# Kernel tuning notes

Hardware: AMD Instinct MI355X
Metric: run time of the kernel (lower is better)

## Reference

```python
import jax, jax.numpy as jnp
import numpy as np

HIDDEN = 1024


def setup_inputs() -> dict:
    key = jax.random.key(0)
    ks = jax.random.split(key, 8)
    x_in, y_in, out_dim, hidden = 1024, 1024, 1024, HIDDEN
    Nx, Ny = 4096, 4096
    s = lambda d: 1.0 / np.sqrt(d)
    return {
        "x": jax.random.normal(ks[0], (Nx, x_in), jnp.float32),
        "y": jax.random.normal(ks[1], (Ny, y_in), jnp.float32),
        "Wq": jax.random.normal(ks[2], (hidden, x_in), jnp.float32) * s(x_in),
        "bq": jnp.zeros((hidden,), jnp.float32),
        "Wk": jax.random.normal(ks[3], (hidden, y_in), jnp.float32) * s(y_in),
        "bk": jnp.zeros((hidden,), jnp.float32),
        "Wv": jax.random.normal(ks[4], (out_dim, y_in), jnp.float32) * s(y_in),
        "bv": jnp.zeros((out_dim,), jnp.float32),
    }


def reference(x, y, Wq, bq, Wk, bk, Wv, bv):
    # Linear projections (torch Linear: x @ W.T + b)
    q = x @ Wq.T + bq          # [Nx, H]
    k = y @ Wk.T + bk          # [Ny, H]
    v = y @ Wv.T + bv          # [Ny, D_out]
    scores = (q @ k.T) / jnp.sqrt(jnp.asarray(HIDDEN, q.dtype))  # [Nx, Ny]
    attn = jax.nn.softmax(scores, axis=1)
    return attn @ v            # [Nx, D_out]
```

## Files before the change

kernel.cpp:

```cpp
#include <hip/hip_runtime.h>
#include <cstdint>
#include <cstddef>

typedef __attribute__((ext_vector_type(8))) __bf16 bf16x8;
typedef __attribute__((ext_vector_type(4))) float  f32x4;

#define WAITCNT_VM(n)   ((n & 0xF) | 0x70 | 0xF00 | (((n) >> 4) << 14))
#define WAITCNT_LGKM(n) (0xF | 0x70 | ((n) << 8) | (3 << 14))

__device__ __forceinline__ unsigned short f32_to_bf16(float f) {
    union { float f; unsigned int u; } cv;
    cv.f = f;
    unsigned int u = cv.u;
    return (unsigned short)((u + 0x7fffu + ((u >> 16) & 1u)) >> 16);
}

__device__ __forceinline__ float bf16_to_f32(unsigned short h) {
    union { unsigned int u; float f; } cv;
    cv.u = ((unsigned int)h) << 16;
    return cv.f;
}

__device__ __forceinline__ void async_copy16(const unsigned short* g, unsigned short* lds) {
    __builtin_amdgcn_global_load_lds(
        (const __attribute__((address_space(1))) unsigned int*)g,
        (__attribute__((address_space(3))) unsigned int*)lds,
        16, 0, 0);
}

__global__ __launch_bounds__(256) void cast_all(
    const float* __restrict__ x,  const float* __restrict__ y,
    const float* __restrict__ wq, const float* __restrict__ wk, const float* __restrict__ wv,
    unsigned short* __restrict__ xb,  unsigned short* __restrict__ yb,
    unsigned short* __restrict__ wqb, unsigned short* __restrict__ wkb,
    unsigned short* __restrict__ wvb, float* __restrict__ lsum)
{
    int b = blockIdx.x;
    if (b >= 11264) {
        float4 z = {0.f, 0.f, 0.f, 0.f};
#pragma unroll
        for (int t = 0; t < 4; ++t)
            ((float4*)lsum)[threadIdx.x * 4 + t] = z;
        return;
    }
    const float* s; unsigned short* d; int base;
    if      (b < 4096)  { s = x;  d = xb;  base = b; }
    else if (b < 8192)  { s = y;  d = yb;  base = b - 4096; }
    else if (b < 9216)  { s = wq; d = wqb; base = b - 8192; }
    else if (b < 10240) { s = wk; d = wkb; base = b - 9216; }
    else                { s = wv; d = wvb; base = b - 10240; }
    int i = base * 256 + threadIdx.x;
    float4 v = ((const float4*)s)[i];
    ushort4 o;
    o.x = f32_to_bf16(v.x);
    o.y = f32_to_bf16(v.y);
    o.z = f32_to_bf16(v.z);
    o.w = f32_to_bf16(v.w);
    ((ushort4*)d)[i] = o;
}

__device__ __forceinline__ void gemm_core_pf(
    const unsigned short* __restrict__ A, const unsigned short* __restrict__ B,
    int K, int rowBase, int colBase, int kBeg, int kEnd,
    unsigned short* ldsA, unsigned short* ldsB, f32x4 acc[4][4])
{
    const int tid  = threadIdx.x;
    const int lane = tid & 63;
    const int wave = tid >> 6;
    const int quad = lane >> 4;
    const int r    = lane & 15;
    const int wm   = wave >> 1;
    const int wn   = wave & 1;

    const int c1 = tid + 256;
    const long aOff0 = (long)(rowBase + (tid >> 2)) * K + (tid & 3) * 8;
    const long aOff1 = (long)(rowBase + (c1  >> 2)) * K + (c1  & 3) * 8;
    const long bOff0 = (long)(colBase + (tid >> 2)) * K + (tid & 3) * 8;
    const long bOff1 = (long)(colBase + (c1  >> 2)) * K + (c1  & 3) * 8;
    unsigned short* ldsA0 = ldsA + tid * 8;
    unsigned short* ldsA1 = ldsA + c1 * 8;
    unsigned short* ldsB0 = ldsB + tid * 8;
    unsigned short* ldsB1 = ldsB + c1 * 8;

    const int aReadOff = (wm * 64 + r) * 32 + quad * 8;
    const int bReadOff = (wn * 64 + r) * 32 + quad * 8;

    const int nSteps = (kEnd - kBeg) >> 5;

    async_copy16(A + aOff0 + kBeg, ldsA0);
    async_copy16(A + aOff1 + kBeg, ldsA1);
    async_copy16(B + bOff0 + kBeg, ldsB0);
    async_copy16(B + bOff1 + kBeg, ldsB1);

    for (int s = 0; s < nSteps; ++s) {
        const int cur = (s & 1) << 12;
        const int nxt = cur ^ 4096;
        __builtin_amdgcn_s_waitcnt(0);
        __syncthreads();
        if (s + 1 < nSteps) {
            const int kn = kBeg + ((s + 1) << 5);
            async_copy16(A + aOff0 + kn, ldsA0 + nxt);
            async_copy16(A + aOff1 + kn, ldsA1 + nxt);
            async_copy16(B + bOff0 + kn, ldsB0 + nxt);
            async_copy16(B + bOff1 + kn, ldsB1 + nxt);
        }
        bf16x8 af[4], bfr[4];
#pragma unroll
        for (int i = 0; i < 4; ++i)
            af[i] = *(const bf16x8*)(ldsA + cur + aReadOff + i * 16 * 32);
#pragma unroll
        for (int j = 0; j < 4; ++j)
            bfr[j] = *(const bf16x8*)(ldsB + cur + bReadOff + j * 16 * 32);
#pragma unroll
        for (int i = 0; i < 4; ++i)
#pragma unroll
            for (int j = 0; j < 4; ++j)
                acc[i][j] = __builtin_amdgcn_mfma_f32_16x16x32_bf16(af[i], bfr[j], acc[i][j], 0, 0, 0);
    }
}

__global__ __launch_bounds__(256, 2)
void proj_batched(const unsigned short* __restrict__ xb, const unsigned short* __restrict__ yb,
                  const unsigned short* __restrict__ wqb, const unsigned short* __restrict__ wkb,
                  const unsigned short* __restrict__ wvb,
                  unsigned short* __restrict__ q, unsigned short* __restrict__ k,
                  unsigned short* __restrict__ vt,
                  const float* __restrict__ bq, const float* __restrict__ bk,
                  const float* __restrict__ bv)
{
    __shared__ __align__(16) unsigned short ldsA[2 * 128 * 32];
    __shared__ __align__(16) unsigned short ldsB[2 * 128 * 32];

    const int b = blockIdx.x;
    const int z = b >> 8;
    const int rb = b & 255;

    const unsigned short *A, *B;
    unsigned short* C;
    const float* bias;
    int N, rowBase, colBase;
    bool biasPerRow;
    if (z == 0) {
        A = xb; B = wqb; C = q; bias = bq; N = 1024; biasPerRow = false;
        colBase = (rb >> 5) * 128; rowBase = (rb & 31) * 128;
    } else if (z == 1) {
        A = yb; B = wkb; C = k; bias = bk; N = 1024; biasPerRow = false;
        colBase = (rb >> 5) * 128; rowBase = (rb & 31) * 128;
    } else {
        A = wvb; B = yb; C = vt; bias = bv; N = 4096; biasPerRow = true;
        colBase = (rb >> 3) * 128; rowBase = (rb & 7) * 128;
    }

    f32x4 acc[4][4];
#pragma unroll
    for (int i = 0; i < 4; ++i)
#pragma unroll
        for (int j = 0; j < 4; ++j)
            acc[i][j] = (f32x4){0.f, 0.f, 0.f, 0.f};

    gemm_core_pf(A, B, 1024, rowBase, colBase, 0, 1024, ldsA, ldsB, acc);

    const int lane = threadIdx.x & 63;
    const int wave = threadIdx.x >> 6;
    const int quad = lane >> 4;
    const int r    = lane & 15;
    const int orow0 = rowBase + (wave >> 1) * 64 + quad * 4;
    const int ocol0 = colBase + (wave & 1) * 64 + r;

#pragma unroll
    for (int i = 0; i < 4; ++i)
#pragma unroll
        for (int e = 0; e < 4; ++e) {
            const int row = orow0 + i * 16 + e;
            const float brow = biasPerRow ? bias[row] : 0.f;
#pragma unroll
            for (int j = 0; j < 4; ++j) {
                const int col = ocol0 + j * 16;
                const float bb = biasPerRow ? brow : bias[col];
                C[(long)row * N + col] = f32_to_bf16(acc[i][j][e] + bb);
            }
        }
}

__device__ __forceinline__ void stage_half(const unsigned short* src, long rstep,
                                           unsigned short* ldsLane) {
    async_copy16(src, ldsLane);
    async_copy16(src + rstep, ldsLane + 4096);
}

__device__ __forceinline__ void gemm256_core(
    const unsigned short* __restrict__ A, const unsigned short* __restrict__ B,
    int K, int rowBase, int colBase, int kBeg, int nTiles,
    unsigned short* lds, f32x4 acc[8][4])
{
    const int tid  = threadIdx.x;
    const int lane = tid & 63;
    const int wid  = tid >> 6;
    const int quad = lane >> 4;
    const int r    = lane & 15;
    const int wm   = wid >> 2;
    const int wn   = wid & 3;

    const int row0 = tid >> 3;
    const int chs8 = (((tid & 7) ^ (row0 & 7)) << 3);
    const unsigned short* As = A + (long)(rowBase + row0) * K + chs8 + kBeg;
    const unsigned short* Bs = B + (long)(colBase + row0) * K + chs8 + kBeg;
    const long rstep = (long)K * 64;
    const long hstep = (long)K * 128;
    unsigned short* ldsLane = lds + tid * 8;

    const int aRd = (wm << 13) + (r << 6);
    const int bRd = 16384 + (wn << 12) + (r << 6);
    const int sw0 = ((quad ^ (r & 7)) << 3);
    const int sw1 = (((quad + 4) ^ (r & 7)) << 3);

    stage_half(As,         rstep, ldsLane);
    stage_half(As + hstep, rstep, ldsLane + 8192);
    stage_half(Bs,         rstep, ldsLane + 16384);
    stage_half(Bs + hstep, rstep, ldsLane + 24576);
    if (nTiles > 1) {
        stage_half(Bs + 64,         rstep, ldsLane + 32768 + 16384);
        stage_half(Bs + hstep + 64, rstep, ldsLane + 32768 + 24576);
    }
    __builtin_amdgcn_s_waitcnt(WAITCNT_VM(4));
    __builtin_amdgcn_s_barrier();
    __builtin_amdgcn_sched_barrier(0);

    bf16x8 aE[4], aO[4], bX[4], bY[4];
#pragma unroll
    for (int i = 0; i < 4; ++i)
        aE[i] = *(const bf16x8*)(lds + aRd + i * 1024 + sw0);
#pragma unroll
    for (int j = 0; j < 4; ++j)
        bX[j] = *(const bf16x8*)(lds + bRd + j * 1024 + sw0);

    for (int T = 0; T < nTiles; ++T) {
        const int cur = (T & 1) << 15;
        const int nxt = cur ^ 32768;

#pragma unroll
        for (int i = 0; i < 4; ++i)
            aO[i] = *(const bf16x8*)(lds + cur + aRd + (4 + i) * 1024 + sw0);
        __builtin_amdgcn_s_waitcnt(WAITCNT_LGKM(4));
        __builtin_amdgcn_sched_barrier(0);
        __builtin_amdgcn_s_setprio(1);
#pragma unroll
        for (int i = 0; i < 4; ++i)
#pragma unroll
            for (int j = 0; j < 4; ++j)
                acc[i][j] = __builtin_amdgcn_mfma_f32_16x16x32_bf16(aE[i], bX[j], acc[i][j], 0, 0, 0);
        __builtin_amdgcn_s_setprio(0);
        __builtin_amdgcn_sched_barrier(0);
        __builtin_amdgcn_s_barrier();
        if (T + 1 < nTiles) stage_half(As + (T + 1) * 64, rstep, ldsLane + nxt);

#pragma unroll
        for (int i = 0; i < 4; ++i)
            aE[i] = *(const bf16x8*)(lds + cur + aRd + i * 1024 + sw1);
#pragma unroll
        for (int j = 0; j < 4; ++j)
            bY[j] = *(const bf16x8*)(lds + cur + bRd + j * 1024 + sw1);
        __builtin_amdgcn_s_waitcnt(WAITCNT_LGKM(8));
        __builtin_amdgcn_sched_barrier(0);
        __builtin_amdgcn_s_setprio(1);
#pragma unroll
        for (int i = 0; i < 4; ++i)
#pragma unroll
            for (int j = 0; j < 4; ++j)
                acc[4 + i][j] = __builtin_amdgcn_mfma_f32_16x16x32_bf16(aO[i], bX[j], acc[4 + i][j], 0, 0, 0);
        __builtin_amdgcn_s_setprio(0);
        __builtin_amdgcn_sched_barrier(0);
        __builtin_amdgcn_s_barrier();
        if (T + 1 < nTiles) stage_half(As + hstep + (T + 1) * 64, rstep, ldsLane + nxt + 8192);

#pragma unroll
        for (int i = 0; i < 4; ++i)
            aO[i] = *(const bf16x8*)(lds + cur + aRd + (4 + i) * 1024 + sw1);
        __builtin_amdgcn_s_waitcnt(WAITCNT_LGKM(4));
        __builtin_amdgcn_sched_barrier(0);
        __builtin_amdgcn_s_setprio(1);
#pragma unroll
        for (int i = 0; i < 4; ++i)
#pragma unroll
            for (int j = 0; j < 4; ++j)
                acc[i][j] = __builtin_amdgcn_mfma_f32_16x16x32_bf16(aE[i], bY[j], acc[i][j], 0, 0, 0);
        __builtin_amdgcn_s_setprio(0);
        __builtin_amdgcn_sched_barrier(0);
        __builtin_amdgcn_s_barrier();
        if (T + 2 < nTiles) stage_half(Bs + (T + 2) * 64, rstep, ldsLane + cur + 16384);

        if (T + 1 < nTiles) {
            if (T + 2 < nTiles) __builtin_amdgcn_s_waitcnt(WAITCNT_VM(2));
            else                __builtin_amdgcn_s_waitcnt(WAITCNT_VM(0));
            __builtin_amdgcn_s_barrier();
            __builtin_amdgcn_sched_barrier(0);
#pragma unroll
            for (int i = 0; i < 4; ++i)
                aE[i] = *(const bf16x8*)(lds + nxt + aRd + i * 1024 + sw0);
#pragma unroll
            for (int j = 0; j < 4; ++j)
                bX[j] = *(const bf16x8*)(lds + nxt + bRd + j * 1024 + sw0);
            __builtin_amdgcn_s_waitcnt(WAITCNT_LGKM(8));
        } else {
            __builtin_amdgcn_s_waitcnt(WAITCNT_LGKM(0));
        }
        __builtin_amdgcn_sched_barrier(0);
        __builtin_amdgcn_s_setprio(1);
#pragma unroll
        for (int i = 0; i < 4; ++i)
#pragma unroll
            for (int j = 0; j < 4; ++j)
                acc[4 + i][j] = __builtin_amdgcn_mfma_f32_16x16x32_bf16(aO[i], bY[j], acc[4 + i][j], 0, 0, 0);
        __builtin_amdgcn_s_setprio(0);
        __builtin_amdgcn_sched_barrier(0);
        if (T + 2 < nTiles) stage_half(Bs + hstep + (T + 2) * 64, rstep, ldsLane + cur + 24576);
    }
}

__global__ __launch_bounds__(512, 2)
void scores_gemm256(const unsigned short* __restrict__ q, const unsigned short* __restrict__ k,
                    unsigned short* __restrict__ P, float* __restrict__ lsum, float scale2)
{
    __shared__ __align__(16) unsigned short lds[2 * 32768];

    const int bid = blockIdx.x;
    const int swz = (bid & 7) * 32 + (bid >> 3);
    const int mt = swz >> 4, nt = swz & 15;
    const int rowBase = mt * 256;
    const int colBase = nt * 256;

    f32x4 acc[8][4];
#pragma unroll
    for (int i = 0; i < 8; ++i)
#pragma unroll
        for (int j = 0; j < 4; ++j)
            acc[i][j] = (f32x4){0.f, 0.f, 0.f, 0.f};

    gemm256_core(q, k, 1024, rowBase, colBase, 0, 16, lds, acc);

    const int lane = threadIdx.x & 63;
    const int wid  = threadIdx.x >> 6;
    const int quad = lane >> 4;
    const int r    = lane & 15;
    const int orow0 = rowBase + (wid >> 2) * 128 + quad * 4;
    const int ocol0 = colBase + (wid & 3) * 64 + r;

#pragma unroll
    for (int mi = 0; mi < 8; ++mi)
#pragma unroll
        for (int e = 0; e < 4; ++e) {
            const int row = orow0 + mi * 16 + e;
            float rs = 0.f;
#pragma unroll
            for (int nj = 0; nj < 4; ++nj) {
                const float p = exp2f(acc[mi][nj][e] * scale2);
                rs += p;
                P[(long)row * 4096 + ocol0 + nj * 16] = f32_to_bf16(p);
            }
#pragma unroll
            for (int m = 1; m < 16; m <<= 1) rs += __shfl_xor(rs, m, 64);
            if (r == 0) atomicAdd(&lsum[row], rs);
        }
}

template <int ATOMIC>
__global__ __launch_bounds__(512, 2)
void out_gemm256(const unsigned short* __restrict__ P, const unsigned short* __restrict__ vt,
                 void* __restrict__ Out)
{
    __shared__ __align__(16) unsigned short lds[2 * 32768];

    const int bid = blockIdx.x;
    const int swz = (bid & 7) * 32 + (bid >> 3);
    const int z  = swz & 3;
    const int nt = (swz >> 2) & 3;
    const int mt = swz >> 4;
    const int rowBase = mt * 256;
    const int colBase = nt * 256;
    const int kBeg = z * 1024;

    f32x4 acc[8][4];
#pragma unroll
    for (int i = 0; i < 8; ++i)
#pragma unroll
        for (int j = 0; j < 4; ++j)
            acc[i][j] = (f32x4){0.f, 0.f, 0.f, 0.f};

    gemm256_core(P, vt, 4096, rowBase, colBase, kBeg, 16, lds, acc);

    const int lane = threadIdx.x & 63;
    const int wid  = threadIdx.x >> 6;
    const int quad = lane >> 4;
    const int r    = lane & 15;
    const int orow0 = rowBase + (wid >> 2) * 128 + quad * 4;
    const int ocol0 = colBase + (wid & 3) * 64 + r;

#pragma unroll
    for (int mi = 0; mi < 8; ++mi)
#pragma unroll
        for (int e = 0; e < 4; ++e) {
            const int row = orow0 + mi * 16 + e;
#pragma unroll
            for (int nj = 0; nj < 4; ++nj) {
                const int col = ocol0 + nj * 16;
                if (ATOMIC) {
                    atomicAdd(&((float*)Out)[(long)row * 1024 + col], acc[mi][nj][e]);
                } else {
                    unsigned short* parts = (unsigned short*)Out + (size_t)z * (4096 * 1024);
                    parts[(long)row * 1024 + col] = f32_to_bf16(acc[mi][nj][e]);
                }
            }
        }
}

__global__ __launch_bounds__(256) void reduce_norm4(const unsigned short* __restrict__ parts,
                                                    const float* __restrict__ lsum,
                                                    float* __restrict__ O) {
    const int i = blockIdx.x * 256 + threadIdx.x;
    const float inv = 1.0f / lsum[i >> 8];
    const size_t stride = (size_t)(4096 * 1024) / 4;
    ushort4 a = ((const ushort4*)parts)[i];
    ushort4 b = ((const ushort4*)parts)[i + stride];
    ushort4 c = ((const ushort4*)parts)[i + 2 * stride];
    ushort4 d = ((const ushort4*)parts)[i + 3 * stride];
    float4 o;
    o.x = (bf16_to_f32(a.x) + bf16_to_f32(b.x) + bf16_to_f32(c.x) + bf16_to_f32(d.x)) * inv;
    o.y = (bf16_to_f32(a.y) + bf16_to_f32(b.y) + bf16_to_f32(c.y) + bf16_to_f32(d.y)) * inv;
    o.z = (bf16_to_f32(a.z) + bf16_to_f32(b.z) + bf16_to_f32(c.z) + bf16_to_f32(d.z)) * inv;
    o.w = (bf16_to_f32(a.w) + bf16_to_f32(b.w) + bf16_to_f32(c.w) + bf16_to_f32(d.w)) * inv;
    ((float4*)O)[i] = o;
}

__global__ __launch_bounds__(256) void norm_rows(float* __restrict__ O, const float* __restrict__ lsum) {
    int i = blockIdx.x * 256 + threadIdx.x;
    const float inv = 1.0f / lsum[i >> 8];
    float4 v = ((const float4*)O)[i];
    v.x *= inv; v.y *= inv; v.z *= inv; v.w *= inv;
    ((float4*)O)[i] = v;
}

extern "C" void kernel_launch(void* const* d_in, const int* in_sizes, int n_in,
                              void* d_out, int out_size, void* d_ws, size_t ws_size,
                              hipStream_t stream) {
    const float* x  = (const float*)d_in[0];
    const float* y  = (const float*)d_in[1];
    const float* Wq = (const float*)d_in[2];
    const float* bq = (const float*)d_in[3];
    const float* Wk = (const float*)d_in[4];
    const float* bk = (const float*)d_in[5];
    const float* Wv = (const float*)d_in[6];
    const float* bv = (const float*)d_in[7];

    constexpr int Nx = 4096, Ny = 4096, H = 1024, Dv = 1024, Kin = 1024;

    char* ws = (char*)d_ws;
    size_t off = 0;
    auto carve = [&](size_t bytes) {
        char* p = ws + off;
        off += (bytes + 255) & ~(size_t)255;
        return p;
    };

    unsigned short* q_bf  = (unsigned short*)carve((size_t)Nx * H * 2);
    unsigned short* k_bf  = (unsigned short*)carve((size_t)Ny * H * 2);
    unsigned short* vt_bf = (unsigned short*)carve((size_t)Dv * Ny * 2);
    float*          lsum  = (float*)carve((size_t)Nx * sizeof(float));

    char* overlay = ws + off;
    unsigned short* x_bf  = (unsigned short*)overlay;
    unsigned short* y_bf  = x_bf  + (size_t)Nx * Kin;
    unsigned short* Wq_bf = y_bf  + (size_t)Ny * Kin;
    unsigned short* Wk_bf = Wq_bf + (size_t)H  * Kin;
    unsigned short* Wv_bf = Wk_bf + (size_t)H  * Kin;
    unsigned short* P_bf  = (unsigned short*)overlay;

    const size_t overlay_bytes = (size_t)Nx * Ny * 2;
    const size_t partsBytes = (size_t)Nx * Dv * 2;
    unsigned short* parts = (unsigned short*)(overlay + overlay_bytes);
    const size_t need_parts = (size_t)((overlay + overlay_bytes + 4 * partsBytes) - ws);
    const bool useParts = ws_size >= need_parts;

    if (!useParts)
        hipMemsetAsync(d_out, 0, (size_t)Nx * Dv * sizeof(float), stream);

    cast_all<<<11265, 256, 0, stream>>>(x, y, Wq, Wk, Wv, x_bf, y_bf, Wq_bf, Wk_bf, Wv_bf, lsum);

    proj_batched<<<768, 256, 0, stream>>>(x_bf, y_bf, Wq_bf, Wk_bf, Wv_bf,
                                          q_bf, k_bf, vt_bf, bq, bk, bv);

    const float scale2 = 1.4426950408889634f / 32.0f;
    scores_gemm256<<<256, 512, 0, stream>>>(q_bf, k_bf, P_bf, lsum, scale2);

    if (useParts) {
        out_gemm256<0><<<256, 512, 0, stream>>>(P_bf, vt_bf, parts);
        reduce_norm4<<<(Nx * Dv / 4) / 256, 256, 0, stream>>>(parts, lsum, (float*)d_out);
    } else {
        out_gemm256<1><<<256, 512, 0, stream>>>(P_bf, vt_bf, d_out);
        norm_rows<<<Nx * Dv / 4 / 256, 256, 0, stream>>>((float*)d_out, lsum);
    }
}
```

Baseline: 223.1 us.

## Fuse split-K reduction and normalization into output GEMM via last-block counter

Removes the separate reduce_norm4 kernel. Each split-K block of the output GEMM writes its bf16 partial, then increments a per-tile atomic counter, and the last of the four blocks sums the partials, applies the row normalization and writes fp32 output. This saves one kernel launch and lets the reduction overlap with other tiles' GEMM work. In exchange it adds a memset for the counters, fences, and a serialized reduction tail in the last block of each tile.

```diff
diff --git a/kernel.cpp b/kernel.cpp
--- a/kernel.cpp
+++ b/kernel.cpp
@@ -182,13 +182,12 @@
         }
 }
 
-__device__ __forceinline__ void stage_half(const unsigned short* src, long rstep,
-                                           unsigned short* ldsLane) {
-    async_copy16(src, ldsLane);
-    async_copy16(src + rstep, ldsLane + 4096);
-}
-
-__device__ __forceinline__ void gemm256_core(
+#define G256_BAR  __builtin_amdgcn_s_barrier()
+#define G256_SB   __builtin_amdgcn_sched_barrier(0)
+#define G256_PR1  __builtin_amdgcn_s_setprio(1)
+#define G256_PR0  __builtin_amdgcn_s_setprio(0)
+
+__device__ __forceinline__ void gemm256_la(
     const unsigned short* __restrict__ A, const unsigned short* __restrict__ B,
     int K, int rowBase, int colBase, int kBeg, int nTiles,
     unsigned short* lds, f32x4 acc[8][4])
@@ -214,17 +213,22 @@
     const int sw0 = ((quad ^ (r & 7)) << 3);
     const int sw1 = (((quad + 4) ^ (r & 7)) << 3);
 
-    stage_half(As,         rstep, ldsLane);
-    stage_half(As + hstep, rstep, ldsLane + 8192);
-    stage_half(Bs,         rstep, ldsLane + 16384);
-    stage_half(Bs + hstep, rstep, ldsLane + 24576);
+    auto STG = [&](const unsigned short* src, int ldsOff) {
+        async_copy16(src,         ldsLane + ldsOff);
+        async_copy16(src + rstep, ldsLane + ldsOff + 4096);
+    };
+
+    STG(As,         0);
+    STG(As + hstep, 8192);
+    STG(Bs,         16384);
+    STG(Bs + hstep, 24576);
     if (nTiles > 1) {
-        stage_half(Bs + 64,         rstep, ldsLane + 32768 + 16384);
-        stage_half(Bs + hstep + 64, rstep, ldsLane + 32768 + 24576);
+        STG(Bs + 64,         32768 + 16384);
+        STG(Bs + hstep + 64, 32768 + 24576);
     }
     __builtin_amdgcn_s_waitcnt(WAITCNT_VM(4));
-    __builtin_amdgcn_s_barrier();
-    __builtin_amdgcn_sched_barrier(0);
+    G256_BAR;
+    G256_SB;
 
     bf16x8 aE[4], aO[4], bX[4], bY[4];
 #pragma unroll
@@ -242,17 +246,17 @@
         for (int i = 0; i < 4; ++i)
             aO[i] = *(const bf16x8*)(lds + cur + aRd + (4 + i) * 1024 + sw0);
         __builtin_amdgcn_s_waitcnt(WAITCNT_LGKM(4));
-        __builtin_amdgcn_sched_barrier(0);
-        __builtin_amdgcn_s_setprio(1);
+        G256_SB;
+        G256_PR1;
 #pragma unroll
         for (int i = 0; i < 4; ++i)
 #pragma unroll
             for (int j = 0; j < 4; ++j)
                 acc[i][j] = __builtin_amdgcn_mfma_f32_16x16x32_bf16(aE[i], bX[j], acc[i][j], 0, 0, 0);
-        __builtin_amdgcn_s_setprio(0);
-        __builtin_amdgcn_sched_barrier(0);
-        __builtin_amdgcn_s_barrier();
-        if (T + 1 < nTiles) stage_half(As + (T + 1) * 64, rstep, ldsLane + nxt);
+        G256_PR0;
+        G256_SB;
+        G256_BAR;
+        if (T + 1 < nTiles) STG(As + (T + 1) * 64, nxt);
 
 #pragma unroll
         for (int i = 0; i < 4; ++i)
@@ -261,39 +265,39 @@
         for (int j = 0; j < 4; ++j)
             bY[j] = *(const bf16x8*)(lds + cur + bRd + j * 1024 + sw1);
         __builtin_amdgcn_s_waitcnt(WAITCNT_LGKM(8));
-        __builtin_amdgcn_sched_barrier(0);
-        __builtin_amdgcn_s_setprio(1);
+        G256_SB;
+        G256_PR1;
 #pragma unroll
         for (int i = 0; i < 4; ++i)
 #pragma unroll
             for (int j = 0; j < 4; ++j)
                 acc[4 + i][j] = __builtin_amdgcn_mfma_f32_16x16x32_bf16(aO[i], bX[j], acc[4 + i][j], 0, 0, 0);
-        __builtin_amdgcn_s_setprio(0);
-        __builtin_amdgcn_sched_barrier(0);
-        __builtin_amdgcn_s_barrier();
-        if (T + 1 < nTiles) stage_half(As + hstep + (T + 1) * 64, rstep, ldsLane + nxt + 8192);
+        G256_PR0;
+        G256_SB;
+        G256_BAR;
+        if (T + 1 < nTiles) STG(As + hstep + (T + 1) * 64, nxt + 8192);
 
 #pragma unroll
         for (int i = 0; i < 4; ++i)
             aO[i] = *(const bf16x8*)(lds + cur + aRd + (4 + i) * 1024 + sw1);
         __builtin_amdgcn_s_waitcnt(WAITCNT_LGKM(4));
-        __builtin_amdgcn_sched_barrier(0);
-        __builtin_amdgcn_s_setprio(1);
+        G256_SB;
+        G256_PR1;
 #pragma unroll
         for (int i = 0; i < 4; ++i)
 #pragma unroll
             for (int j = 0; j < 4; ++j)
                 acc[i][j] = __builtin_amdgcn_mfma_f32_16x16x32_bf16(aE[i], bY[j], acc[i][j], 0, 0, 0);
-        __builtin_amdgcn_s_setprio(0);
-        __builtin_amdgcn_sched_barrier(0);
-        __builtin_amdgcn_s_barrier();
-        if (T + 2 < nTiles) stage_half(Bs + (T + 2) * 64, rstep, ldsLane + cur + 16384);
+        G256_PR0;
+        G256_SB;
+        G256_BAR;
+        if (T + 2 < nTiles) STG(Bs + (T + 2) * 64, cur + 16384);
 
         if (T + 1 < nTiles) {
             if (T + 2 < nTiles) __builtin_amdgcn_s_waitcnt(WAITCNT_VM(2));
             else                __builtin_amdgcn_s_waitcnt(WAITCNT_VM(0));
-            __builtin_amdgcn_s_barrier();
-            __builtin_amdgcn_sched_barrier(0);
+            G256_BAR;
+            G256_SB;
 #pragma unroll
             for (int i = 0; i < 4; ++i)
                 aE[i] = *(const bf16x8*)(lds + nxt + aRd + i * 1024 + sw0);
@@ -304,16 +308,16 @@
         } else {
             __builtin_amdgcn_s_waitcnt(WAITCNT_LGKM(0));
         }
-        __builtin_amdgcn_sched_barrier(0);
-        __builtin_amdgcn_s_setprio(1);
+        G256_SB;
+        G256_PR1;
 #pragma unroll
         for (int i = 0; i < 4; ++i)
 #pragma unroll
             for (int j = 0; j < 4; ++j)
                 acc[4 + i][j] = __builtin_amdgcn_mfma_f32_16x16x32_bf16(aO[i], bY[j], acc[4 + i][j], 0, 0, 0);
-        __builtin_amdgcn_s_setprio(0);
-        __builtin_amdgcn_sched_barrier(0);
-        if (T + 2 < nTiles) stage_half(Bs + hstep + (T + 2) * 64, rstep, ldsLane + cur + 24576);
+        G256_PR0;
+        G256_SB;
+        if (T + 2 < nTiles) STG(Bs + hstep + (T + 2) * 64, cur + 24576);
     }
 }
 
@@ -336,7 +340,7 @@
         for (int j = 0; j < 4; ++j)
             acc[i][j] = (f32x4){0.f, 0.f, 0.f, 0.f};
 
-    gemm256_core(q, k, 1024, rowBase, colBase, 0, 16, lds, acc);
+    gemm256_la(q, k, 1024, rowBase, colBase, 0, 16, lds, acc);
 
     const int lane = threadIdx.x & 63;
     const int wid  = threadIdx.x >> 6;
@@ -363,12 +367,13 @@
         }
 }
 
-template <int ATOMIC>
 __global__ __launch_bounds__(512, 2)
-void out_gemm256(const unsigned short* __restrict__ P, const unsigned short* __restrict__ vt,
-                 void* __restrict__ Out)
+void out_gemm256_fused(const unsigned short* __restrict__ P, const unsigned short* __restrict__ vt,
+                       unsigned short* __restrict__ parts, const float* __restrict__ lsum,
+                       float* __restrict__ O, unsigned int* __restrict__ cnt)
 {
     __shared__ __align__(16) unsigned short lds[2 * 32768];
+    __shared__ unsigned int sOld;
 
     const int bid = blockIdx.x;
     const int swz = (bid & 7) * 32 + (bid >> 3);
@@ -386,7 +391,7 @@
         for (int j = 0; j < 4; ++j)
             acc[i][j] = (f32x4){0.f, 0.f, 0.f, 0.f};
 
-    gemm256_core(P, vt, 4096, rowBase, colBase, kBeg, 16, lds, acc);
+    gemm256_la(P, vt, 4096, rowBase, colBase, kBeg, 16, lds, acc);
 
     const int lane = threadIdx.x & 63;
     const int wid  = threadIdx.x >> 6;
@@ -395,40 +400,78 @@
     const int orow0 = rowBase + (wid >> 2) * 128 + quad * 4;
     const int ocol0 = colBase + (wid & 3) * 64 + r;
 
+    unsigned short* part = parts + (size_t)z * (4096 * 1024);
 #pragma unroll
     for (int mi = 0; mi < 8; ++mi)
 #pragma unroll
         for (int e = 0; e < 4; ++e) {
             const int row = orow0 + mi * 16 + e;
 #pragma unroll
-            for (int nj = 0; nj < 4; ++nj) {
-                const int col = ocol0 + nj * 16;
-                if (ATOMIC) {
-                    atomicAdd(&((float*)Out)[(long)row * 1024 + col], acc[mi][nj][e]);
-                } else {
-                    unsigned short* parts = (unsigned short*)Out + (size_t)z * (4096 * 1024);
-                    parts[(long)row * 1024 + col] = f32_to_bf16(acc[mi][nj][e]);
-                }
-            }
-        }
-}
-
-__global__ __launch_bounds__(256) void reduce_norm4(const unsigned short* __restrict__ parts,
-                                                    const float* __restrict__ lsum,
-                                                    float* __restrict__ O) {
-    const int i = blockIdx.x * 256 + threadIdx.x;
-    const float inv = 1.0f / lsum[i >> 8];
-    const size_t stride = (size_t)(4096 * 1024) / 4;
-    ushort4 a = ((const ushort4*)parts)[i];
-    ushort4 b = ((const ushort4*)parts)[i + stride];
-    ushort4 c = ((const ushort4*)parts)[i + 2 * stride];
-    ushort4 d = ((const ushort4*)parts)[i + 3 * stride];
-    float4 o;
-    o.x = (bf16_to_f32(a.x) + bf16_to_f32(b.x) + bf16_to_f32(c.x) + bf16_to_f32(d.x)) * inv;
-    o.y = (bf16_to_f32(a.y) + bf16_to_f32(b.y) + bf16_to_f32(c.y) + bf16_to_f32(d.y)) * inv;
-    o.z = (bf16_to_f32(a.z) + bf16_to_f32(b.z) + bf16_to_f32(c.z) + bf16_to_f32(d.z)) * inv;
-    o.w = (bf16_to_f32(a.w) + bf16_to_f32(b.w) + bf16_to_f32(c.w) + bf16_to_f32(d.w)) * inv;
-    ((float4*)O)[i] = o;
+            for (int nj = 0; nj < 4; ++nj)
+                part[(long)row * 1024 + ocol0 + nj * 16] = f32_to_bf16(acc[mi][nj][e]);
+        }
+
+    __syncthreads();
+    if (threadIdx.x == 0) {
+        __threadfence();
+        sOld = __hip_atomic_fetch_add(&cnt[mt * 4 + nt], 1u,
+                                      __ATOMIC_ACQ_REL, __HIP_MEMORY_SCOPE_AGENT);
+    }
+    __syncthreads();
+    if (sOld == 3u) {
+        __threadfence();
+        const size_t stride = 1048576;
+        for (int idx = threadIdx.x; idx < 256 * 64; idx += 512) {
+            const int rrow = idx >> 6;
+            const int c4   = idx & 63;
+            const long i = (long)(rowBase + rrow) * 256 + (colBase >> 2) + c4;
+            const float inv = 1.0f / lsum[rowBase + rrow];
+            ushort4 a = ((const ushort4*)parts)[i];
+            ushort4 b = ((const ushort4*)parts)[i + stride];
+            ushort4 c = ((const ushort4*)parts)[i + 2 * stride];
+            ushort4 d = ((const ushort4*)parts)[i + 3 * stride];
+            float4 o;
+            o.x = (bf16_to_f32(a.x) + bf16_to_f32(b.x) + bf16_to_f32(c.x) + bf16_to_f32(d.x)) * inv;
+            o.y = (bf16_to_f32(a.y) + bf16_to_f32(b.y) + bf16_to_f32(c.y) + bf16_to_f32(d.y)) * inv;
+            o.z = (bf16_to_f32(a.z) + bf16_to_f32(b.z) + bf16_to_f32(c.z) + bf16_to_f32(d.z)) * inv;
+            o.w = (bf16_to_f32(a.w) + bf16_to_f32(b.w) + bf16_to_f32(c.w) + bf16_to_f32(d.w)) * inv;
+            ((float4*)O)[i] = o;
+        }
+    }
+}
+
+__global__ __launch_bounds__(512, 2)
+void out_gemm256_atomic(const unsigned short* __restrict__ P, const unsigned short* __restrict__ vt,
+                        float* __restrict__ Out)
+{
+    __shared__ __align__(16) unsigned short lds[2 * 32768];
+    const int bid = blockIdx.x;
+    const int swz = (bid & 7) * 32 + (bid >> 3);
+    const int z  = swz & 3;
+    const int nt = (swz >> 2) & 3;
+    const int mt = swz >> 4;
+    const int rowBase = mt * 256;
+    const int colBase = nt * 256;
+    f32x4 acc[8][4];
+#pragma unroll
+    for (int i = 0; i < 8; ++i)
+#pragma unroll
+        for (int j = 0; j < 4; ++j)
+            acc[i][j] = (f32x4){0.f, 0.f, 0.f, 0.f};
+    gemm256_la(P, vt, 4096, rowBase, colBase, z * 1024, 16, lds, acc);
+    const int lane = threadIdx.x & 63;
+    const int wid  = threadIdx.x >> 6;
+    const int orow0 = rowBase + (wid >> 2) * 128 + (lane >> 4) * 4;
+    const int ocol0 = colBase + (wid & 3) * 64 + (lane & 15);
+#pragma unroll
+    for (int mi = 0; mi < 8; ++mi)
+#pragma unroll
+        for (int e = 0; e < 4; ++e) {
+            const int row = orow0 + mi * 16 + e;
+#pragma unroll
+            for (int nj = 0; nj < 4; ++nj)
+                atomicAdd(&Out[(long)row * 1024 + ocol0 + nj * 16], acc[mi][nj][e]);
+        }
 }
 
 __global__ __launch_bounds__(256) void norm_rows(float* __restrict__ O, const float* __restrict__ lsum) {
@@ -461,6 +504,7 @@
         return p;
     };
 
+    unsigned int*   cnt   = (unsigned int*)carve(256);
     unsigned short* q_bf  = (unsigned short*)carve((size_t)Nx * H * 2);
     unsigned short* k_bf  = (unsigned short*)carve((size_t)Ny * H * 2);
     unsigned short* vt_bf = (unsigned short*)carve((size_t)Dv * Ny * 2);
@@ -480,22 +524,23 @@
     const size_t need_parts = (size_t)((overlay + overlay_bytes + 4 * partsBytes) - ws);
     const bool useParts = ws_size >= need_parts;
 
-    if (!useParts)
-        hipMemsetAsync(d_out, 0, (size_t)Nx * Dv * sizeof(float), stream);
-
-    cast_all<<<11265, 256, 0, stream>>>(x, y, Wq, Wk, Wv, x_bf, y_bf, Wq_bf, Wk_bf, Wv_bf, lsum);
-
-    proj_batched<<<768, 256, 0, stream>>>(x_bf, y_bf, Wq_bf, Wk_bf, Wv_bf,
-                                          q_bf, k_bf, vt_bf, bq, bk, bv);
-
     const float scale2 = 1.4426950408889634f / 32.0f;
-    scores_gemm256<<<256, 512, 0, stream>>>(q_bf, k_bf, P_bf, lsum, scale2);
+    float* outF = (float*)d_out;
 
     if (useParts) {
-        out_gemm256<0><<<256, 512, 0, stream>>>(P_bf, vt_bf, parts);
-        reduce_norm4<<<(Nx * Dv / 4) / 256, 256, 0, stream>>>(parts, lsum, (float*)d_out);
+        (void)hipMemsetAsync(cnt, 0, 256, stream);
+        cast_all<<<11265, 256, 0, stream>>>(x, y, Wq, Wk, Wv, x_bf, y_bf, Wq_bf, Wk_bf, Wv_bf, lsum);
+        proj_batched<<<768, 256, 0, stream>>>(x_bf, y_bf, Wq_bf, Wk_bf, Wv_bf,
+                                              q_bf, k_bf, vt_bf, bq, bk, bv);
+        scores_gemm256<<<256, 512, 0, stream>>>(q_bf, k_bf, P_bf, lsum, scale2);
+        out_gemm256_fused<<<256, 512, 0, stream>>>(P_bf, vt_bf, parts, lsum, outF, cnt);
     } else {
-        out_gemm256<1><<<256, 512, 0, stream>>>(P_bf, vt_bf, d_out);
-        norm_rows<<<Nx * Dv / 4 / 256, 256, 0, stream>>>((float*)d_out, lsum);
-    }
-}
+        (void)hipMemsetAsync(d_out, 0, (size_t)Nx * Dv * sizeof(float), stream);
+        cast_all<<<11265, 256, 0, stream>>>(x, y, Wq, Wk, Wv, x_bf, y_bf, Wq_bf, Wk_bf, Wv_bf, lsum);
+        proj_batched<<<768, 256, 0, stream>>>(x_bf, y_bf, Wq_bf, Wk_bf, Wv_bf,
+                                              q_bf, k_bf, vt_bf, bq, bk, bv);
+        scores_gemm256<<<256, 512, 0, stream>>>(q_bf, k_bf, P_bf, lsum, scale2);
+        out_gemm256_atomic<<<256, 512, 0, stream>>>(P_bf, vt_bf, outF);
+        norm_rows<<<Nx * Dv / 4 / 256, 256, 0, stream>>>(outF, lsum);
+    }
+}
```

After: 259.5 us. 16.3% more time.
